# Kernel tuning notes

Measured on AMD Instinct MI355X. Metric: run time of the kernel, lower is better.

The kernel has to match this reference:

```python
import jax, jax.numpy as jnp
import numpy as np

D_MODEL = 1024
N_HEADS = 16
N_KV = 4
HEAD_DIM = D_MODEL // N_HEADS
B, T, CACHE_LEN = 2, 1024, 1024
MAX_SEQ = 4096
ROPE_BASE = 10000.0


def _rope_tables(max_seq_len=MAX_SEQ, head_dim=HEAD_DIM, base=ROPE_BASE):
    inv_freq = 1.0 / (base ** (np.arange(0, head_dim, 2, dtype=np.float32) / head_dim))
    t = np.arange(max_seq_len, dtype=np.float32)
    freqs = np.outer(t, inv_freq)                      # [S, hd/2]
    emb = np.concatenate([freqs, freqs], axis=-1)      # [S, hd]
    return jnp.asarray(np.cos(emb)), jnp.asarray(np.sin(emb))


def _rotate_half(x):
    x1, x2 = jnp.split(x, 2, axis=-1)
    return jnp.concatenate([-x2, x1], axis=-1)


def setup_inputs() -> dict:
    key = jax.random.key(0)
    ks = jax.random.split(key, 8)
    return {
        "x": jax.random.normal(ks[0], (B, T, D_MODEL), dtype=jnp.float32),
        "k_cache": jax.random.normal(ks[1], (B, N_KV, CACHE_LEN, HEAD_DIM), dtype=jnp.float32),
        "v_cache": jax.random.normal(ks[2], (B, N_KV, CACHE_LEN, HEAD_DIM), dtype=jnp.float32),
        "position_indices": jax.random.randint(ks[3], (B, T), 0, 1024, dtype=jnp.int32),
        "Wq": jax.random.normal(ks[4], (D_MODEL, D_MODEL), dtype=jnp.float32) * 0.02,
        "Wk": jax.random.normal(ks[5], (D_MODEL, N_KV * HEAD_DIM), dtype=jnp.float32) * 0.02,
        "Wv": jax.random.normal(ks[6], (D_MODEL, N_KV * HEAD_DIM), dtype=jnp.float32) * 0.02,
        "Wo": jax.random.normal(ks[7], (D_MODEL, D_MODEL), dtype=jnp.float32) * 0.02,
    }


def reference(x, k_cache, v_cache, position_indices, Wq, Wk, Wv, Wo):
    Bq, Tq, C = x.shape
    n_kv, cache_len, hd = k_cache.shape[1], k_cache.shape[2], k_cache.shape[3]
    n_heads = Wq.shape[1] // hd
    n_rep = n_heads // n_kv
    scale = hd ** -0.5

    cos, sin = _rope_tables()

    # projections -> [B, H, T, hd]
    q = (x @ Wq).reshape(Bq, Tq, n_heads, hd).transpose(0, 2, 1, 3)
    k = (x @ Wk).reshape(Bq, Tq, n_kv, hd).transpose(0, 2, 1, 3)
    v = (x @ Wv).reshape(Bq, Tq, n_kv, hd).transpose(0, 2, 1, 3)

    # progress-aware RoPE: position-indexed gather into tables, offset by cache len
    offset = cache_len
    t_seq = jnp.arange(Tq, dtype=jnp.int32)[None, :] + offset          # [1, T]
    idx = jnp.clip(position_indices.astype(jnp.int32) + t_seq, 0, cos.shape[0] - 1)  # [B, T]
    cos_b = cos[idx][:, None]  # [B, 1, T, hd]
    sin_b = sin[idx][:, None]
    q = q * cos_b + _rotate_half(q) * sin_b
    k = k * cos_b + _rotate_half(k) * sin_b

    # KV-cache concat
    k = jnp.concatenate([k_cache, k], axis=2)  # [B, n_kv, S, hd]
    v = jnp.concatenate([v_cache, v], axis=2)

    # GQA head expansion (repeat each kv head n_rep times, contiguous grouping)
    k_exp = jnp.repeat(k, n_rep, axis=1)  # [B, H, S, hd]
    v_exp = jnp.repeat(v, n_rep, axis=1)

    # manual attention path (k_cache provided -> NO causal mask, matching torch code)
    attn = jnp.einsum("bhtd,bhsd->bhts", q, k_exp) * scale
    attn = jax.nn.softmax(attn, axis=-1)
    out = jnp.einsum("bhts,bhsd->bhtd", attn, v_exp)
    out = out.transpose(0, 2, 1, 3).reshape(Bq, Tq, C)
    return out @ Wo, k, v
```

## Files before the change

### kernel.cpp

```cpp
#include <hip/hip_runtime.h>
#include <hip/hip_bf16.h>
#include <stdint.h>

#define D_MODEL 1024
#define N_HEADS 16
#define N_KV 4
#define HD 64
#define BB 2
#define TT 1024
#define CACHE_LEN 1024
#define SS 2048
#define MAX_SEQ 4096
#define QKV_N 1536
#define NROWS 32768
#define GRP_EL (SS * HD)
#define NSP 4

typedef __attribute__((ext_vector_type(8))) short bf16x8;
typedef __attribute__((ext_vector_type(4))) float f32x4;

__device__ inline short f2bs(float f) {
    __hip_bfloat16 h = __float2bfloat16(f);
    return *reinterpret_cast<short*>(&h);
}
__device__ inline float bs2f(short s) {
    return __uint_as_float((unsigned)(unsigned short)s << 16);
}

__device__ inline int kfrag_off(int s, int d) {
    return (s >> 4) * 1024 + ((d >= 32) ? 512 : 0) + ((((d & 31) >> 3) * 16 + (s & 15)) * 8) + (d & 7);
}
__device__ inline int vfrag_off(int s, int d) {
    return ((s >> 5) * 4 + (d >> 4)) * 512 + ((((s >> 2) & 3) * 16 + (d & 15)) * 8)
         + (((s >> 4) & 1) * 4) + (s & 3);
}

__device__ void transp_body(const float* __restrict__ src, short* __restrict__ dst,
                            int N, int bx, int by) {
    __shared__ short tile[32][34];
    int tx = threadIdx.x & 31, ty = threadIdx.x >> 5;
    int n0 = bx * 32, k0 = by * 32;
#pragma unroll
    for (int i = 0; i < 4; i++)
        tile[ty + i * 8][tx] = f2bs(src[(size_t)(k0 + ty + i * 8) * N + n0 + tx]);
    __syncthreads();
#pragma unroll
    for (int i = 0; i < 4; i++)
        dst[(size_t)(n0 + ty + i * 8) * 1024 + k0 + tx] = tile[tx][ty + i * 8];
}

__global__ void k_prep(const float* __restrict__ x, short* __restrict__ xb,
                       const float* __restrict__ Wq, const float* __restrict__ Wk,
                       const float* __restrict__ Wv, const float* __restrict__ Wo,
                       short* __restrict__ Wt, short* __restrict__ Wot) {
    int id = blockIdx.x;
    if (id < 2048) {
        int i = (id * 256 + threadIdx.x) * 4;
        float4 v = *reinterpret_cast<const float4*>(x + i);
        short4 o = make_short4(f2bs(v.x), f2bs(v.y), f2bs(v.z), f2bs(v.w));
        *reinterpret_cast<short4*>(xb + i) = o;
        return;
    }
    id -= 2048;
    if (id < 1024) { transp_body(Wq, Wt, 1024, id & 31, id >> 5); return; }
    id -= 1024;
    if (id < 256)  { transp_body(Wk, Wt + (size_t)1024 * 1024, 256, id & 7, id >> 3); return; }
    id -= 256;
    if (id < 256)  { transp_body(Wv, Wt + (size_t)1280 * 1024, 256, id & 7, id >> 3); return; }
    id -= 256;
    transp_body(Wo, Wot, 1024, id & 31, id >> 5);
}

template <bool BF16_OUT>
__global__ __launch_bounds__(256) void k_gemm64(
    const short* __restrict__ A, const short* __restrict__ Bt, void* __restrict__ Cv,
    int M, int N, int K) {
    __shared__ short sA[2][64 * 32];
    __shared__ short sB[2][64 * 32];
    int m0 = blockIdx.y * 64, n0 = blockIdx.x * 64;
    int g = threadIdx.x;
    int lane = g & 63, wave = g >> 6;
    int wr = wave >> 1, wc = wave & 1;
    int quad = lane >> 4, l15 = lane & 15;

    f32x4 acc[2][2] = {};

    for (int k0 = 0; k0 < K; k0 += 64) {
        __syncthreads();
#pragma unroll
        for (int i = 0; i < 2; i++) {
            int cb = wave * 2 + i;
            int h = cb >> 2, c = cb & 3;
            int row = c * 16 + (lane >> 2);
            int kcol = k0 + h * 32 + (lane & 3) * 8;
            const short* srcA = A + (size_t)(m0 + row) * K + kcol;
            const short* srcB = Bt + (size_t)(n0 + row) * K + kcol;
            __builtin_amdgcn_global_load_lds(
                (const __attribute__((address_space(1))) void*)srcA,
                (__attribute__((address_space(3))) void*)((char*)&sA[h][0] + c * 1024), 16, 0, 0);
            __builtin_amdgcn_global_load_lds(
                (const __attribute__((address_space(1))) void*)srcB,
                (__attribute__((address_space(3))) void*)((char*)&sB[h][0] + c * 1024), 16, 0, 0);
        }
        __syncthreads();
#pragma unroll
        for (int h = 0; h < 2; h++) {
            bf16x8 af[2], bfr[2];
#pragma unroll
            for (int i = 0; i < 2; i++)
                af[i] = *reinterpret_cast<const bf16x8*>(&sA[h][(wr * 32 + i * 16 + l15) * 32 + quad * 8]);
#pragma unroll
            for (int j = 0; j < 2; j++)
                bfr[j] = *reinterpret_cast<const bf16x8*>(&sB[h][(wc * 32 + j * 16 + l15) * 32 + quad * 8]);
#pragma unroll
            for (int i = 0; i < 2; i++)
#pragma unroll
                for (int j = 0; j < 2; j++)
                    acc[i][j] = __builtin_amdgcn_mfma_f32_16x16x32_bf16(af[i], bfr[j], acc[i][j], 0, 0, 0);
        }
    }
#pragma unroll
    for (int i = 0; i < 2; i++) {
        int m = m0 + wr * 32 + i * 16 + quad * 4;
#pragma unroll
        for (int j = 0; j < 2; j++) {
            int n = n0 + wc * 32 + j * 16 + l15;
#pragma unroll
            for (int r = 0; r < 4; r++) {
                if constexpr (BF16_OUT)
                    ((short*)Cv)[(size_t)(m + r) * N + n] = f2bs(acc[i][j][r]);
                else
                    ((float*)Cv)[(size_t)(m + r) * N + n] = acc[i][j][r];
            }
        }
    }
}

__global__ void k_post(const short* __restrict__ qkvb, const int* __restrict__ pos,
                       const float* __restrict__ k_cache, const float* __restrict__ v_cache,
                       short* __restrict__ qb, short* __restrict__ kf, short* __restrict__ vf,
                       float* __restrict__ k_out, float* __restrict__ v_out) {
    int id = blockIdx.x;
    if (id < 2048) {
        int row = id;
        int b = row >> 10, t = row & 1023;
        int g = threadIdx.x;
        __shared__ float scv[32], ssv[32];
        if (g < 32) {
            int idx = pos[row] + t + CACHE_LEN;
            idx = min(max(idx, 0), MAX_SEQ - 1);
            float inv = expf(-(float)g * (9.210340371976184f / 32.0f));
            sincosf((float)idx * inv, &ssv[g], &scv[g]);
        }
        __syncthreads();
        const short* src = qkvb + (size_t)row * QKV_N;
        const float QS = 0.18033688011112042f;
#pragma unroll
        for (int p = g; p < 512; p += 256) {
            int h = p >> 5, i = p & 31;
            float cv = scv[i], sv = ssv[i];
            float x1 = bs2f(src[h * 64 + i]), x2 = bs2f(src[h * 64 + i + 32]);
            size_t qbase = ((size_t)(b * N_HEADS + h) * TT + t) * HD;
            qb[qbase + i]      = f2bs((x1 * cv - x2 * sv) * QS);
            qb[qbase + i + 32] = f2bs((x2 * cv + x1 * sv) * QS);
        }
        if (g < 128) {
            int h = g >> 5, i = g & 31;
            float cv = scv[i], sv = ssv[i];
            float x1 = bs2f(src[1024 + h * 64 + i]), x2 = bs2f(src[1024 + h * 64 + i + 32]);
            float o1 = x1 * cv - x2 * sv;
            float o2 = x2 * cv + x1 * sv;
            int s = CACHE_LEN + t;
            size_t kbase = ((size_t)(b * N_KV + h) * SS + s) * HD;
            k_out[kbase + i] = o1;
            k_out[kbase + i + 32] = o2;
            short* kfb = kf + (size_t)(b * N_KV + h) * GRP_EL;
            kfb[kfrag_off(s, i)]      = f2bs(o1);
            kfb[kfrag_off(s, i + 32)] = f2bs(o2);
        }
        return;
    }
    int i = (id - 2048) * 256 + threadIdx.x;
    int d = i & 63;
    int s = (i >> 6) & 2047;
    int bh = i >> 17;
    int b = bh >> 2, h = bh & 3;
    if (s < CACHE_LEN) {
        size_t cidx = ((size_t)bh * CACHE_LEN + s) * HD + d;
        size_t oidx = ((size_t)bh * SS + s) * HD + d;
        float kv = k_cache[cidx];
        float vv = v_cache[cidx];
        k_out[oidx] = kv;
        v_out[oidx] = vv;
        kf[(size_t)bh * GRP_EL + kfrag_off(s, d)] = f2bs(kv);
        vf[(size_t)bh * GRP_EL + vfrag_off(s, d)] = f2bs(vv);
    } else {
        short vb = qkvb[(size_t)(b * TT + (s - CACHE_LEN)) * QKV_N + 1280 + h * 64 + d];
        v_out[((size_t)bh * SS + s) * HD + d] = bs2f(vb);
        vf[(size_t)bh * GRP_EL + vfrag_off(s, d)] = vb;
    }
}

__global__ __launch_bounds__(256, 4) void k_attn(
    const short* __restrict__ qb, const short* __restrict__ kf, const short* __restrict__ vf,
    ushort* __restrict__ po, float* __restrict__ pl) {
    __shared__ short tile[8192];
    int bx = blockIdx.x;
    int sp = bx >> 5;
    int bh = bx & 31;
    int b = bh >> 4, h = bh & 15;
    int hkv = h >> 2;
    int lane = threadIdx.x & 63, wave = threadIdx.x >> 6;
    int quad = lane >> 4, l15 = lane & 15;
    int tw0 = blockIdx.y * 128 + wave * 16;
    int tw1 = tw0 + 64;

    const short* qrow0 = qb + ((size_t)bh * TT + tw0 + l15) * HD;
    const short* qrow1 = qb + ((size_t)bh * TT + tw1 + l15) * HD;
    bf16x8 aq00 = *reinterpret_cast<const bf16x8*>(qrow0 + quad * 8);
    bf16x8 aq01 = *reinterpret_cast<const bf16x8*>(qrow0 + 32 + quad * 8);
    bf16x8 aq10 = *reinterpret_cast<const bf16x8*>(qrow1 + quad * 8);
    bf16x8 aq11 = *reinterpret_cast<const bf16x8*>(qrow1 + 32 + quad * 8);

    const short* kfb = kf + (size_t)(b * N_KV + hkv) * GRP_EL;
    const short* vfb = vf + (size_t)(b * N_KV + hkv) * GRP_EL;

    f32x4 o0[4] = {}, o1[4] = {};
    float lr0 = 0.f, lr1 = 0.f;

    int sbeg = sp * (SS / NSP);
    for (int s0 = sbeg; s0 < sbeg + SS / NSP; s0 += 64) {
        __syncthreads();
#pragma unroll
        for (int i = 0; i < 4; i++) {
            int ch = wave * 4 + i;
            const short* src = (ch < 8)
                ? kfb + (s0 >> 4) * 1024 + ch * 512 + lane * 8
                : vfb + (s0 >> 5) * 2048 + (ch - 8) * 512 + lane * 8;
            __builtin_amdgcn_global_load_lds(
                (const __attribute__((address_space(1))) void*)src,
                (__attribute__((address_space(3))) void*)((char*)tile + ch * 1024), 16, 0, 0);
        }
        __syncthreads();

#pragma unroll
        for (int pp = 0; pp < 2; pp++) {
            f32x4 s0c[2], s1c[2];
#pragma unroll
            for (int ti = 0; ti < 2; ti++) {
                int nt = pp * 2 + ti;
                bf16x8 ak0 = *reinterpret_cast<const bf16x8*>(tile + nt * 1024 + lane * 8);
                bf16x8 ak1 = *reinterpret_cast<const bf16x8*>(tile + nt * 1024 + 512 + lane * 8);
                f32x4 z = {};
                z = __builtin_amdgcn_mfma_f32_16x16x32_bf16(ak0, aq00, z, 0, 0, 0);
                z = __builtin_amdgcn_mfma_f32_16x16x32_bf16(ak1, aq01, z, 0, 0, 0);
                s0c[ti] = z;
                f32x4 w = {};
                w = __builtin_amdgcn_mfma_f32_16x16x32_bf16(ak0, aq10, w, 0, 0, 0);
                w = __builtin_amdgcn_mfma_f32_16x16x32_bf16(ak1, aq11, w, 0, 0, 0);
                s1c[ti] = w;
            }
            bf16x8 bp0, bp1;
#pragma unroll
            for (int ti = 0; ti < 2; ti++)
#pragma unroll
                for (int r = 0; r < 4; r++) {
                    float p0 = exp2f(s0c[ti][r]);
                    float p1 = exp2f(s1c[ti][r]);
                    lr0 += p0;
                    lr1 += p1;
                    bp0[ti * 4 + r] = f2bs(p0);
                    bp1[ti * 4 + r] = f2bs(p1);
                }
#pragma unroll
            for (int dt = 0; dt < 4; dt++) {
                bf16x8 av = *reinterpret_cast<const bf16x8*>(
                    tile + 4096 + (pp * 4 + dt) * 512 + lane * 8);
                o0[dt] = __builtin_amdgcn_mfma_f32_16x16x32_bf16(av, bp0, o0[dt], 0, 0, 0);
                o1[dt] = __builtin_amdgcn_mfma_f32_16x16x32_bf16(av, bp1, o1[dt], 0, 0, 0);
            }
        }
    }

    lr0 += __shfl_xor(lr0, 16);
    lr0 += __shfl_xor(lr0, 32);
    lr1 += __shfl_xor(lr1, 16);
    lr1 += __shfl_xor(lr1, 32);

    size_t row0 = (size_t)bh * TT + tw0 + l15;
    size_t row1 = (size_t)bh * TT + tw1 + l15;
    if (quad == 0) {
        pl[(size_t)sp * NROWS + row0] = lr0;
        pl[(size_t)sp * NROWS + row1] = lr1;
    }
#pragma unroll
    for (int dt = 0; dt < 4; dt++) {
        ushort4 w0, w1;
        w0.x = (ushort)f2bs(o0[dt][0]); w0.y = (ushort)f2bs(o0[dt][1]);
        w0.z = (ushort)f2bs(o0[dt][2]); w0.w = (ushort)f2bs(o0[dt][3]);
        w1.x = (ushort)f2bs(o1[dt][0]); w1.y = (ushort)f2bs(o1[dt][1]);
        w1.z = (ushort)f2bs(o1[dt][2]); w1.w = (ushort)f2bs(o1[dt][3]);
        *reinterpret_cast<ushort4*>(po + ((size_t)sp * NROWS + row0) * 64 + dt * 16 + quad * 4) = w0;
        *reinterpret_cast<ushort4*>(po + ((size_t)sp * NROWS + row1) * 64 + dt * 16 + quad * 4) = w1;
    }
}

__global__ void k_merge(const ushort* __restrict__ po, const float* __restrict__ pl,
                        short* __restrict__ ob) {
    int g = threadIdx.x;
    int row = blockIdx.x * 16 + (g >> 4);
    int d0 = (g & 15) * 4;
    float l = 0.f;
#pragma unroll
    for (int sp = 0; sp < NSP; sp++) l += pl[(size_t)sp * NROWS + row];
    float a0 = 0, a1 = 0, a2 = 0, a3 = 0;
#pragma unroll
    for (int sp = 0; sp < NSP; sp++) {
        ushort4 u = *reinterpret_cast<const ushort4*>(po + ((size_t)sp * NROWS + row) * 64 + d0);
        a0 += __uint_as_float((unsigned)u.x << 16);
        a1 += __uint_as_float((unsigned)u.y << 16);
        a2 += __uint_as_float((unsigned)u.z << 16);
        a3 += __uint_as_float((unsigned)u.w << 16);
    }
    float inv = 1.0f / l;
    int bh = row >> 10, t = row & 1023;
    int b = bh >> 4, h = bh & 15;
    short4 w = make_short4(f2bs(a0 * inv), f2bs(a1 * inv), f2bs(a2 * inv), f2bs(a3 * inv));
    *reinterpret_cast<short4*>(ob + (size_t)(b * TT + t) * D_MODEL + h * 64 + d0) = w;
}

extern "C" void kernel_launch(void* const* d_in, const int* in_sizes, int n_in,
                              void* d_out, int out_size, void* d_ws, size_t ws_size,
                              hipStream_t stream) {
    (void)in_sizes; (void)n_in; (void)out_size; (void)ws_size;
    const float* x       = (const float*)d_in[0];
    const float* k_cache = (const float*)d_in[1];
    const float* v_cache = (const float*)d_in[2];
    const int*   pos     = (const int*)d_in[3];
    const float* Wq      = (const float*)d_in[4];
    const float* Wk      = (const float*)d_in[5];
    const float* Wv      = (const float*)d_in[6];
    const float* Wo      = (const float*)d_in[7];

    float* out   = (float*)d_out;
    float* k_out = out + (size_t)BB * TT * D_MODEL;
    float* v_out = k_out + (size_t)BB * N_KV * SS * HD;

    char* ws = (char*)d_ws;
    short* qkvb = (short*)(ws);
    short* xb   = (short*)(ws + (6u << 20));
    short* Wt   = (short*)(ws + (10u << 20));
    short* qbuf = (short*)(ws + (15u << 20));
    short* kfr  = (short*)(ws + (19u << 20));
    short* vfr  = (short*)(ws + (21u << 20));
    short* obuf = (short*)(ws + (23u << 20));
    short* Wot  = (short*)(ws + (27u << 20));
    float* pl   = (float*)(ws + (29u << 20));
    ushort* po  = (ushort*)(ws);

    k_prep<<<4608, 256, 0, stream>>>(x, xb, Wq, Wk, Wv, Wo, Wt, Wot);

    k_gemm64<true><<<dim3(QKV_N / 64, 2048 / 64), 256, 0, stream>>>(
        xb, Wt, qkvb, 2048, QKV_N, 1024);

    k_post<<<6144, 256, 0, stream>>>(qkvb, pos, k_cache, v_cache,
                                     qbuf, kfr, vfr, k_out, v_out);

    k_attn<<<dim3(32 * NSP, TT / 128), 256, 0, stream>>>(qbuf, kfr, vfr, po, pl);
    k_merge<<<2048, 256, 0, stream>>>(po, pl, obuf);

    k_gemm64<false><<<dim3(1024 / 64, 2048 / 64), 256, 0, stream>>>(
        obuf, Wot, (float*)d_out, 2048, 1024, 1024);
}
```

Measured before the change: 153.1 us.

## Fuse RoPE and KV scatter into QKV GEMM epilogue, move cache copy to prep

Removes the separate k_post kernel. The QKV GEMM now stages its fp32 accumulators in LDS and applies RoPE, Q scaling, and the K/V fragment scatter directly in the epilogue. Cos/sin tables and the cache copy into k_out/v_out and the bf16 fragments move into the prep kernel. This drops one launch and the round trip of the bf16 QKV intermediate, and RoPE now uses unrounded fp32 values. The attention split count also drops from 4 to 2, which trades fewer partials to merge for less parallelism in k_attn.

```diff
diff --git a/kernel.cpp b/kernel.cpp
--- a/kernel.cpp
+++ b/kernel.cpp
@@ -14,7 +14,7 @@
 #define QKV_N 1536
 #define NROWS 32768
 #define GRP_EL (SS * HD)
-#define NSP 4
+#define NSP 2
 
 typedef __attribute__((ext_vector_type(8))) short bf16x8;
 typedef __attribute__((ext_vector_type(4))) float f32x4;
@@ -52,10 +52,16 @@
 __global__ void k_prep(const float* __restrict__ x, short* __restrict__ xb,
                        const float* __restrict__ Wq, const float* __restrict__ Wk,
                        const float* __restrict__ Wv, const float* __restrict__ Wo,
-                       short* __restrict__ Wt, short* __restrict__ Wot) {
+                       short* __restrict__ Wt, short* __restrict__ Wot,
+                       const float* __restrict__ k_cache, const float* __restrict__ v_cache,
+                       float* __restrict__ k_out, float* __restrict__ v_out,
+                       short* __restrict__ kf, short* __restrict__ vf,
+                       const int* __restrict__ pos,
+                       float* __restrict__ costab, float* __restrict__ sintab) {
     int id = blockIdx.x;
+    int g = threadIdx.x;
     if (id < 2048) {
-        int i = (id * 256 + threadIdx.x) * 4;
+        int i = (id * 256 + g) * 4;
         float4 v = *reinterpret_cast<const float4*>(x + i);
         short4 o = make_short4(f2bs(v.x), f2bs(v.y), f2bs(v.z), f2bs(v.w));
         *reinterpret_cast<short4*>(xb + i) = o;
@@ -68,12 +74,143 @@
     id -= 256;
     if (id < 256)  { transp_body(Wv, Wt + (size_t)1280 * 1024, 256, id & 7, id >> 3); return; }
     id -= 256;
-    transp_body(Wo, Wot, 1024, id & 31, id >> 5);
-}
-
-template <bool BF16_OUT>
+    if (id < 1024) { transp_body(Wo, Wot, 1024, id & 31, id >> 5); return; }
+    id -= 1024;
+    if (id < 2048) {
+        int i = id * 256 + g;
+        int d = i & 63;
+        int s = (i >> 6) & 1023;
+        int bh = i >> 16;
+        size_t cidx = ((size_t)bh * CACHE_LEN + s) * HD + d;
+        size_t oidx = ((size_t)bh * SS + s) * HD + d;
+        float kv = k_cache[cidx];
+        float vv = v_cache[cidx];
+        k_out[oidx] = kv;
+        v_out[oidx] = vv;
+        kf[(size_t)bh * GRP_EL + kfrag_off(s, d)] = f2bs(kv);
+        vf[(size_t)bh * GRP_EL + vfrag_off(s, d)] = f2bs(vv);
+        return;
+    }
+    id -= 2048;
+    {
+        int p = id * 256 + g;
+        int row = p >> 5, i = p & 31;
+        int idx = pos[row] + (row & 1023) + CACHE_LEN;
+        idx = min(max(idx, 0), MAX_SEQ - 1);
+        float inv = expf(-(float)i * (9.210340371976184f / 32.0f));
+        float sv, cv;
+        sincosf((float)idx * inv, &sv, &cv);
+        costab[p] = cv;
+        sintab[p] = sv;
+    }
+}
+
+__global__ __launch_bounds__(256) void k_gemm_qkv(
+    const short* __restrict__ A, const short* __restrict__ Bt,
+    const float* __restrict__ costab, const float* __restrict__ sintab,
+    short* __restrict__ qb, short* __restrict__ kf, short* __restrict__ vf,
+    float* __restrict__ k_out, float* __restrict__ v_out) {
+    __shared__ float eplds[64 * 65];
+    short* sA = (short*)eplds;
+    short* sB = sA + 4096;
+    int m0 = blockIdx.y * 64, n0 = blockIdx.x * 64;
+    int g = threadIdx.x;
+    int lane = g & 63, wave = g >> 6;
+    int wr = wave >> 1, wc = wave & 1;
+    int quad = lane >> 4, l15 = lane & 15;
+
+    f32x4 acc[2][2] = {};
+
+    for (int k0 = 0; k0 < 1024; k0 += 64) {
+        __syncthreads();
+#pragma unroll
+        for (int i = 0; i < 2; i++) {
+            int cb = wave * 2 + i;
+            int h = cb >> 2, c = cb & 3;
+            int row = c * 16 + (lane >> 2);
+            int kcol = k0 + h * 32 + (lane & 3) * 8;
+            const short* srcA = A + (size_t)(m0 + row) * 1024 + kcol;
+            const short* srcB = Bt + (size_t)(n0 + row) * 1024 + kcol;
+            __builtin_amdgcn_global_load_lds(
+                (const __attribute__((address_space(1))) void*)srcA,
+                (__attribute__((address_space(3))) void*)((char*)sA + h * 4096 + c * 1024), 16, 0, 0);
+            __builtin_amdgcn_global_load_lds(
+                (const __attribute__((address_space(1))) void*)srcB,
+                (__attribute__((address_space(3))) void*)((char*)sB + h * 4096 + c * 1024), 16, 0, 0);
+        }
+        __syncthreads();
+#pragma unroll
+        for (int h = 0; h < 2; h++) {
+            bf16x8 af[2], bfr[2];
+#pragma unroll
+            for (int i = 0; i < 2; i++)
+                af[i] = *reinterpret_cast<const bf16x8*>(sA + h * 2048 + (wr * 32 + i * 16 + l15) * 32 + quad * 8);
+#pragma unroll
+            for (int j = 0; j < 2; j++)
+                bfr[j] = *reinterpret_cast<const bf16x8*>(sB + h * 2048 + (wc * 32 + j * 16 + l15) * 32 + quad * 8);
+#pragma unroll
+            for (int i = 0; i < 2; i++)
+#pragma unroll
+                for (int j = 0; j < 2; j++)
+                    acc[i][j] = __builtin_amdgcn_mfma_f32_16x16x32_bf16(af[i], bfr[j], acc[i][j], 0, 0, 0);
+        }
+    }
+    __syncthreads();
+#pragma unroll
+    for (int i = 0; i < 2; i++)
+#pragma unroll
+        for (int j = 0; j < 2; j++)
+#pragma unroll
+            for (int r = 0; r < 4; r++)
+                eplds[(wr * 32 + i * 16 + quad * 4 + r) * 65 + wc * 32 + j * 16 + l15] = acc[i][j][r];
+    __syncthreads();
+
+    int bx = blockIdx.x;
+    const float QS = 0.18033688011112042f;
+    if (bx < 20) {
+#pragma unroll
+        for (int rep = 0; rep < 8; rep++) {
+            int p = rep * 256 + g;
+            int row = p >> 5, i = p & 31;
+            int m = m0 + row;
+            int b = m >> 10, t = m & 1023;
+            float cv = costab[m * 32 + i], sv = sintab[m * 32 + i];
+            float x1 = eplds[row * 65 + i], x2 = eplds[row * 65 + i + 32];
+            float o1 = x1 * cv - x2 * sv;
+            float o2 = x2 * cv + x1 * sv;
+            if (bx < 16) {
+                size_t qbase = ((size_t)(b * N_HEADS + bx) * TT + t) * HD;
+                qb[qbase + i]      = f2bs(o1 * QS);
+                qb[qbase + i + 32] = f2bs(o2 * QS);
+            } else {
+                int h = bx - 16;
+                int s = CACHE_LEN + t;
+                size_t kbase = ((size_t)(b * N_KV + h) * SS + s) * HD;
+                k_out[kbase + i]      = o1;
+                k_out[kbase + i + 32] = o2;
+                short* kfb = kf + (size_t)(b * N_KV + h) * GRP_EL;
+                kfb[kfrag_off(s, i)]      = f2bs(o1);
+                kfb[kfrag_off(s, i + 32)] = f2bs(o2);
+            }
+        }
+    } else {
+        int h = bx - 20;
+#pragma unroll
+        for (int rep = 0; rep < 16; rep++) {
+            int p = rep * 256 + g;
+            int row = p >> 6, d = p & 63;
+            int m = m0 + row;
+            int b = m >> 10, t = m & 1023;
+            int s = CACHE_LEN + t;
+            float val = eplds[row * 65 + d];
+            v_out[((size_t)(b * N_KV + h) * SS + s) * HD + d] = val;
+            vf[(size_t)(b * N_KV + h) * GRP_EL + vfrag_off(s, d)] = f2bs(val);
+        }
+    }
+}
+
 __global__ __launch_bounds__(256) void k_gemm64(
-    const short* __restrict__ A, const short* __restrict__ Bt, void* __restrict__ Cv,
+    const short* __restrict__ A, const short* __restrict__ Bt, float* __restrict__ C,
     int M, int N, int K) {
     __shared__ short sA[2][64 * 32];
     __shared__ short sB[2][64 * 32];
@@ -126,78 +263,9 @@
         for (int j = 0; j < 2; j++) {
             int n = n0 + wc * 32 + j * 16 + l15;
 #pragma unroll
-            for (int r = 0; r < 4; r++) {
-                if constexpr (BF16_OUT)
-                    ((short*)Cv)[(size_t)(m + r) * N + n] = f2bs(acc[i][j][r]);
-                else
-                    ((float*)Cv)[(size_t)(m + r) * N + n] = acc[i][j][r];
-            }
-        }
-    }
-}
-
-__global__ void k_post(const short* __restrict__ qkvb, const int* __restrict__ pos,
-                       const float* __restrict__ k_cache, const float* __restrict__ v_cache,
-                       short* __restrict__ qb, short* __restrict__ kf, short* __restrict__ vf,
-                       float* __restrict__ k_out, float* __restrict__ v_out) {
-    int id = blockIdx.x;
-    if (id < 2048) {
-        int row = id;
-        int b = row >> 10, t = row & 1023;
-        int g = threadIdx.x;
-        __shared__ float scv[32], ssv[32];
-        if (g < 32) {
-            int idx = pos[row] + t + CACHE_LEN;
-            idx = min(max(idx, 0), MAX_SEQ - 1);
-            float inv = expf(-(float)g * (9.210340371976184f / 32.0f));
-            sincosf((float)idx * inv, &ssv[g], &scv[g]);
-        }
-        __syncthreads();
-        const short* src = qkvb + (size_t)row * QKV_N;
-        const float QS = 0.18033688011112042f;
-#pragma unroll
-        for (int p = g; p < 512; p += 256) {
-            int h = p >> 5, i = p & 31;
-            float cv = scv[i], sv = ssv[i];
-            float x1 = bs2f(src[h * 64 + i]), x2 = bs2f(src[h * 64 + i + 32]);
-            size_t qbase = ((size_t)(b * N_HEADS + h) * TT + t) * HD;
-            qb[qbase + i]      = f2bs((x1 * cv - x2 * sv) * QS);
-            qb[qbase + i + 32] = f2bs((x2 * cv + x1 * sv) * QS);
-        }
-        if (g < 128) {
-            int h = g >> 5, i = g & 31;
-            float cv = scv[i], sv = ssv[i];
-            float x1 = bs2f(src[1024 + h * 64 + i]), x2 = bs2f(src[1024 + h * 64 + i + 32]);
-            float o1 = x1 * cv - x2 * sv;
-            float o2 = x2 * cv + x1 * sv;
-            int s = CACHE_LEN + t;
-            size_t kbase = ((size_t)(b * N_KV + h) * SS + s) * HD;
-            k_out[kbase + i] = o1;
-            k_out[kbase + i + 32] = o2;
-            short* kfb = kf + (size_t)(b * N_KV + h) * GRP_EL;
-            kfb[kfrag_off(s, i)]      = f2bs(o1);
-            kfb[kfrag_off(s, i + 32)] = f2bs(o2);
-        }
-        return;
-    }
-    int i = (id - 2048) * 256 + threadIdx.x;
-    int d = i & 63;
-    int s = (i >> 6) & 2047;
-    int bh = i >> 17;
-    int b = bh >> 2, h = bh & 3;
-    if (s < CACHE_LEN) {
-        size_t cidx = ((size_t)bh * CACHE_LEN + s) * HD + d;
-        size_t oidx = ((size_t)bh * SS + s) * HD + d;
-        float kv = k_cache[cidx];
-        float vv = v_cache[cidx];
-        k_out[oidx] = kv;
-        v_out[oidx] = vv;
-        kf[(size_t)bh * GRP_EL + kfrag_off(s, d)] = f2bs(kv);
-        vf[(size_t)bh * GRP_EL + vfrag_off(s, d)] = f2bs(vv);
-    } else {
-        short vb = qkvb[(size_t)(b * TT + (s - CACHE_LEN)) * QKV_N + 1280 + h * 64 + d];
-        v_out[((size_t)bh * SS + s) * HD + d] = bs2f(vb);
-        vf[(size_t)bh * GRP_EL + vfrag_off(s, d)] = vb;
+            for (int r = 0; r < 4; r++)
+                C[(size_t)(m + r) * N + n] = acc[i][j][r];
+        }
     }
 }
 
@@ -347,28 +415,28 @@
     float* v_out = k_out + (size_t)BB * N_KV * SS * HD;
 
     char* ws = (char*)d_ws;
-    short* qkvb = (short*)(ws);
-    short* xb   = (short*)(ws + (6u << 20));
-    short* Wt   = (short*)(ws + (10u << 20));
-    short* qbuf = (short*)(ws + (15u << 20));
-    short* kfr  = (short*)(ws + (19u << 20));
-    short* vfr  = (short*)(ws + (21u << 20));
-    short* obuf = (short*)(ws + (23u << 20));
-    short* Wot  = (short*)(ws + (27u << 20));
-    float* pl   = (float*)(ws + (29u << 20));
-    ushort* po  = (ushort*)(ws);
-
-    k_prep<<<4608, 256, 0, stream>>>(x, xb, Wq, Wk, Wv, Wo, Wt, Wot);
-
-    k_gemm64<true><<<dim3(QKV_N / 64, 2048 / 64), 256, 0, stream>>>(
-        xb, Wt, qkvb, 2048, QKV_N, 1024);
-
-    k_post<<<6144, 256, 0, stream>>>(qkvb, pos, k_cache, v_cache,
-                                     qbuf, kfr, vfr, k_out, v_out);
+    short* xb     = (short*)(ws);
+    short* Wt     = (short*)(ws + (4u << 20));
+    float* costab = (float*)(ws + (7u << 20));
+    float* sintab = (float*)(ws + (7u << 20) + (256u << 10));
+    short* qbuf   = (short*)(ws + (8u << 20));
+    short* kfr    = (short*)(ws + (12u << 20));
+    short* vfr    = (short*)(ws + (14u << 20));
+    short* obuf   = (short*)(ws + (16u << 20));
+    short* Wot    = (short*)(ws + (20u << 20));
+    float* pl     = (float*)(ws + (22u << 20));
+    ushort* po    = (ushort*)(ws);
+
+    k_prep<<<6912, 256, 0, stream>>>(x, xb, Wq, Wk, Wv, Wo, Wt, Wot,
+                                     k_cache, v_cache, k_out, v_out, kfr, vfr,
+                                     pos, costab, sintab);
+
+    k_gemm_qkv<<<dim3(QKV_N / 64, 2048 / 64), 256, 0, stream>>>(
+        xb, Wt, costab, sintab, qbuf, kfr, vfr, k_out, v_out);
 
     k_attn<<<dim3(32 * NSP, TT / 128), 256, 0, stream>>>(qbuf, kfr, vfr, po, pl);
     k_merge<<<2048, 256, 0, stream>>>(po, pl, obuf);
 
-    k_gemm64<false><<<dim3(1024 / 64, 2048 / 64), 256, 0, stream>>>(
+    k_gemm64<<<dim3(1024 / 64, 2048 / 64), 256, 0, stream>>>(
         obuf, Wot, (float*)d_out, 2048, 1024, 1024);
 }
```

Result: faster. 149.4 us (-2.4%).
